# Performance work log

Measured on AMD Instinct MI355X. Metric: run time of the kernel, lower is better.

## Reference

```python
import jax, jax.numpy as jnp
import numpy as np

EPS_BN = 1e-5


def conv2d(x, w, b, stride=1, pad=0):
    y = jax.lax.conv_general_dilated(
        x, w, (stride, stride), [(pad, pad), (pad, pad)],
        dimension_numbers=('NCHW', 'OIHW', 'NCHW'))
    return y + b[None, :, None, None]


def resize_ac(x, oh, ow):
    # bilinear resize, align_corners=True (matches F.interpolate(..., align_corners=True))
    N, C, H, W = x.shape
    ys = jnp.linspace(0.0, H - 1.0, oh)
    xs = jnp.linspace(0.0, W - 1.0, ow)
    y0 = jnp.floor(ys).astype(jnp.int32)
    x0 = jnp.floor(xs).astype(jnp.int32)
    y1 = jnp.minimum(y0 + 1, H - 1)
    x1 = jnp.minimum(x0 + 1, W - 1)
    wy = (ys - y0)[None, None, :, None]
    wx = (xs - x0)[None, None, None, :]
    top = jnp.take(x, y0, axis=2)
    bot = jnp.take(x, y1, axis=2)
    rows = top * (1.0 - wy) + bot * wy
    left = jnp.take(rows, x0, axis=3)
    right = jnp.take(rows, x1, axis=3)
    return left * (1.0 - wx) + right * wx


def grid_sample_3d(vol, grid):
    # vol: (N,C,D,H,W); grid: (N,Do,Ho,Wo,3) with channels (x->W, y->H, z->D)
    # trilinear, padding_mode='zeros', align_corners=False (torch defaults)
    N, C, D, H, W = vol.shape
    out_shape = grid.shape[1:4]
    gx = grid[..., 0].reshape(N, -1)
    gy = grid[..., 1].reshape(N, -1)
    gz = grid[..., 2].reshape(N, -1)
    ix = ((gx + 1.0) * W - 1.0) * 0.5
    iy = ((gy + 1.0) * H - 1.0) * 0.5
    iz = ((gz + 1.0) * D - 1.0) * 0.5
    x0 = jnp.floor(ix); y0 = jnp.floor(iy); z0 = jnp.floor(iz)
    fx = ix - x0; fy = iy - y0; fz = iz - z0
    volf = vol.reshape(N, C, D * H * W)

    def corner(xi, yi, zi, wgt):
        valid = ((xi >= 0) & (xi < W) & (yi >= 0) & (yi < H) & (zi >= 0) & (zi < D))
        xc = jnp.clip(xi, 0, W - 1).astype(jnp.int32)
        yc = jnp.clip(yi, 0, H - 1).astype(jnp.int32)
        zc = jnp.clip(zi, 0, D - 1).astype(jnp.int32)
        lin = (zc * H + yc) * W + xc  # (N,P)
        g = jnp.take_along_axis(volf, lin[:, None, :], axis=2)  # (N,C,P)
        return g * (wgt * valid.astype(vol.dtype))[:, None, :]

    out = 0.0
    for zi, wz in ((z0, 1.0 - fz), (z0 + 1.0, fz)):
        for yi, wy in ((y0, 1.0 - fy), (y0 + 1.0, fy)):
            for xi, wx in ((x0, 1.0 - fx), (x0 + 1.0, fx)):
                out = out + corner(xi, yi, zi, wz * wy * wx)
    return out.reshape(N, C, *out_shape)


def setup_inputs() -> dict:
    key = jax.random.key(0)
    ks = jax.random.split(key, 9)
    N, H, W = 1, 2048, 2048
    f = lambda k, shp, s: jax.random.normal(k, shp, jnp.float32) * s
    return dict(
        low=jax.random.uniform(ks[0], (N, 3, H, W), jnp.float32),
        med=jax.random.uniform(ks[1], (N, 3, H, W), jnp.float32),
        high=jax.random.uniform(ks[2], (N, 3, H, W), jnp.float32),
        w1=f(ks[3], (16, 9, 3, 3), 0.1), b1=jnp.zeros((16,), jnp.float32),
        w2=f(ks[4], (32, 16, 3, 3), 0.1), b2=jnp.zeros((32,), jnp.float32),
        w3=f(ks[5], (64, 32, 3, 3), 0.1), b3=jnp.zeros((64,), jnp.float32),
        w4=f(ks[6], (192, 64, 1, 1), 0.1), b4=jnp.zeros((192,), jnp.float32),
        gw1=f(ks[7], (16, 3, 1, 1), 0.3), gb1=jnp.zeros((16,), jnp.float32),
        g_gamma=jnp.ones((16,), jnp.float32), g_beta=jnp.zeros((16,), jnp.float32),
        g_mean=jnp.zeros((16,), jnp.float32), g_var=jnp.ones((16,), jnp.float32),
        gw2=f(ks[8], (1, 16, 1, 1), 0.3), gb2=jnp.zeros((1,), jnp.float32),
    )


def _forward(low, med, high, w1, b1, w2, b2, w3, b3, w4, b4,
             gw1, gb1, g_gamma, g_beta, g_mean, g_var, gw2, gb2):
    img = 0.33 * low + 0.33 * med + 0.33 * high  # (N,3,H,W)

    # ---- Coeffs: downsample 9-ch input to 128x128, run coeff net -> (N,12,16,16,16)
    x = resize_ac(jnp.concatenate([low, med, high], axis=1), 128, 128)
    x = jax.nn.relu(conv2d(x, w1, b1, stride=2, pad=1))   # 64x64
    x = jax.nn.relu(conv2d(x, w2, b2, stride=2, pad=1))   # 32x32
    x = jax.nn.relu(conv2d(x, w3, b3, stride=2, pad=1))   # 16x16
    coeff = conv2d(x, w4, b4, stride=1, pad=0)            # (N,192,16,16)
    grid_vol = coeff.reshape(-1, 12, 16, 16, 16)          # (N,12,D,H,W)

    # ---- GuideNN at full res: 1x1 conv -> BN(eval) -> ReLU -> 1x1 conv -> sigmoid
    g = conv2d(img, gw1, gb1)
    g = g_gamma[None, :, None, None] * (g - g_mean[None, :, None, None]) \
        * jax.lax.rsqrt(g_var[None, :, None, None] + EPS_BN) + g_beta[None, :, None, None]
    g = jax.nn.relu(g)
    guide = jax.nn.sigmoid(conv2d(g, gw2, gb2))           # (N,1,H,W)
    guide = resize_ac(guide, 64, 64)[:, 0]                # (N,64,64)

    # ---- Slice: trilinear lookup into bilateral grid, guided by (guide, hg, wg)
    N = guide.shape[0]
    lin = (jnp.arange(64, dtype=jnp.float32) / 63.0) * 2.0 - 1.0
    hg = jnp.broadcast_to(lin[:, None], (64, 64))
    wg = jnp.broadcast_to(lin[None, :], (64, 64))
    grid = jnp.stack([guide,
                      jnp.broadcast_to(hg, guide.shape),
                      jnp.broadcast_to(wg, guide.shape)], axis=-1)[:, None]  # (N,1,64,64,3)
    sc = grid_sample_3d(grid_vol, grid)[:, :, 0]          # (N,12,64,64)

    # ---- Apply: upsample coeffs to full res, per-pixel 3x4 affine (HDRNet apply)
    Hi, Wi = img.shape[2], img.shape[3]
    cf = resize_ac(sc, Hi, Wi).reshape(N, 3, 4, Hi, Wi)
    out = jnp.einsum('ncjhw,njhw->nchw', cf[:, :, :3], img) + cf[:, :, 3]
    return out


def reference(low, med, high, w1, b1, w2, b2, w3, b3, w4, b4,
              gw1, gb1, g_gamma, g_beta, g_mean, g_var, gw2, gb2):
    return _forward(low, med, high, w1, b1, w2, b2, w3, b3, w4, b4,
                    gw1, gb1, g_gamma, g_beta, g_mean, g_var, gw2, gb2)
```

## Files before the change

kernel.cpp:

```cpp
#include <hip/hip_runtime.h>
#include <math.h>

#define HH 2048
#define WW 2048
#define HWFULL (HH*WW)

typedef float v4f __attribute__((ext_vector_type(4)));
union F4 { float4 v; v4f c; float f[4]; };

__global__ __launch_bounds__(256) void k_conv1(const float* __restrict__ low,
                                               const float* __restrict__ med,
                                               const float* __restrict__ high,
                                               const float* __restrict__ w,
                                               const float* __restrict__ b,
                                               float* __restrict__ out) {
    __shared__ float sd[9 * 3 * 34];
    const int oy = blockIdx.x >> 2;
    const int q  = blockIdx.x & 3;
    const int tid = threadIdx.x;
    for (int idx = tid; idx < 9 * 3 * 33; idx += 256) {
        int ch = idx / 99;
        int rem = idx - 99 * ch;
        int r = rem / 33;
        int j = rem - 33 * r;
        int ix128 = 32 * q - 1 + j;
        int iy128 = 2 * oy - 1 + r;
        float val = 0.0f;
        if (ix128 >= 0 && ix128 < 128 && iy128 >= 0 && iy128 < 128) {
            const float* base = (ch < 3) ? low : (ch < 6 ? med : high);
            const float* p = base + (ch % 3) * HWFULL;
            float ysf = iy128 * (2047.0f / 127.0f);
            int y0 = (int)ysf; if (y0 > 2047) y0 = 2047;
            int y1 = y0 + 1;   if (y1 > 2047) y1 = 2047;
            float wy = ysf - (float)y0;
            float xsf = ix128 * (2047.0f / 127.0f);
            int x0 = (int)xsf; if (x0 > 2047) x0 = 2047;
            int x1 = x0 + 1;   if (x1 > 2047) x1 = 2047;
            float wx = xsf - (float)x0;
            float t = p[y0 * WW + x0] * (1.0f - wx) + p[y0 * WW + x1] * wx;
            float bo = p[y1 * WW + x0] * (1.0f - wx) + p[y1 * WW + x1] * wx;
            val = t * (1.0f - wy) + bo * wy;
        }
        sd[(ch * 3 + r) * 34 + j] = val;
    }
    __syncthreads();
    int co = tid >> 4, xl = tid & 15;
    float acc = b[co];
    for (int ci = 0; ci < 9; ++ci) {
        #pragma unroll
        for (int ky = 0; ky < 3; ++ky) {
            const float* wr = w + ((co * 9 + ci) * 3 + ky) * 3;
            const float* row = &sd[(ci * 3 + ky) * 34 + 2 * xl];
            acc += wr[0] * row[0] + wr[1] * row[1] + wr[2] * row[2];
        }
    }
    out[co * 4096 + oy * 64 + 16 * q + xl] = fmaxf(acc, 0.0f);
}

__global__ __launch_bounds__(256) void k_conv2(const float* __restrict__ in,
                                               const float* __restrict__ w,
                                               const float* __restrict__ b,
                                               const float* __restrict__ low,
                                               const float* __restrict__ med,
                                               const float* __restrict__ high,
                                               const float* __restrict__ gw1, const float* __restrict__ gb1,
                                               const float* __restrict__ gamma, const float* __restrict__ beta,
                                               const float* __restrict__ mean, const float* __restrict__ var,
                                               const float* __restrict__ gw2, const float* __restrict__ gb2,
                                               float* __restrict__ out,
                                               float* __restrict__ guideb) {
    __shared__ float sd[16 * 3 * 18];
    const int oy = blockIdx.x >> 2;
    const int q  = blockIdx.x & 3;
    const int tid = threadIdx.x;
    for (int idx = tid; idx < 16 * 3 * 17; idx += 256) {
        int ch = idx / 51;
        int rem = idx - 51 * ch;
        int r = rem / 17;
        int j = rem - 17 * r;
        int x = 16 * q - 1 + j;
        int iy = 2 * oy - 1 + r;
        sd[(ch * 3 + r) * 18 + j] =
            (x >= 0 && x < 64 && iy >= 0 && iy < 64) ? in[ch * 4096 + iy * 64 + x] : 0.0f;
    }
    __syncthreads();
    int co = tid >> 3, xl = tid & 7;
    float acc = b[co];
    for (int ci = 0; ci < 16; ++ci) {
        #pragma unroll
        for (int ky = 0; ky < 3; ++ky) {
            const float* wr = w + ((co * 16 + ci) * 3 + ky) * 3;
            const float* row = &sd[(ci * 3 + ky) * 18 + 2 * xl];
            acc += wr[0] * row[0] + wr[1] * row[1] + wr[2] * row[2];
        }
    }
    out[co * 1024 + oy * 32 + 8 * q + xl] = fmaxf(acc, 0.0f);

    if (tid < 32) {
        int g = blockIdx.x * 32 + tid;
        int h = g >> 6, wv = g & 63;
        float ysf = h * (2047.0f / 63.0f);
        int y0 = (int)ysf; if (y0 > 2047) y0 = 2047;
        int y1 = y0 + 1;   if (y1 > 2047) y1 = 2047;
        float wy = ysf - (float)y0;
        float xsf = wv * (2047.0f / 63.0f);
        int x0 = (int)xsf; if (x0 > 2047) x0 = 2047;
        int x1 = x0 + 1;   if (x1 > 2047) x1 = 2047;
        float wx = xsf - (float)x0;
        int yy[2] = { y0, y1 };
        int xx[2] = { x0, x1 };
        float gp[2][2];
        #pragma unroll
        for (int a = 0; a < 2; ++a) {
            #pragma unroll
            for (int bb = 0; bb < 2; ++bb) {
                int pix = yy[a] * WW + xx[bb];
                float i0 = 0.33f * (low[pix]            + med[pix]            + high[pix]);
                float i1 = 0.33f * (low[HWFULL + pix]   + med[HWFULL + pix]   + high[HWFULL + pix]);
                float i2 = 0.33f * (low[2*HWFULL + pix] + med[2*HWFULL + pix] + high[2*HWFULL + pix]);
                float acc2 = gb2[0];
                for (int k = 0; k < 16; ++k) {
                    float t = gb1[k] + gw1[k*3] * i0 + gw1[k*3+1] * i1 + gw1[k*3+2] * i2;
                    t = gamma[k] * (t - mean[k]) * (1.0f / sqrtf(var[k] + 1e-5f)) + beta[k];
                    t = fmaxf(t, 0.0f);
                    acc2 += gw2[k] * t;
                }
                gp[a][bb] = 1.0f / (1.0f + expf(-acc2));
            }
        }
        guideb[g] = (1.0f - wy) * ((1.0f - wx) * gp[0][0] + wx * gp[0][1])
                  +         wy  * ((1.0f - wx) * gp[1][0] + wx * gp[1][1]);
    }
}

__global__ __launch_bounds__(256) void k_conv34(const float* __restrict__ in,
                                                const float* __restrict__ w3,
                                                const float* __restrict__ b3,
                                                const float* __restrict__ w4,
                                                const float* __restrict__ b4,
                                                float* __restrict__ gridvol) {
    __shared__ float sd[32 * 3 * 10];
    __shared__ float sc3[64 * 4];
    const int oy = blockIdx.x >> 2;
    const int q  = blockIdx.x & 3;
    const int tid = threadIdx.x;
    for (int idx = tid; idx < 32 * 3 * 9; idx += 256) {
        int ch = idx / 27;
        int rem = idx - 27 * ch;
        int r = rem / 9;
        int j = rem - 9 * r;
        int x = 8 * q - 1 + j;
        int iy = 2 * oy - 1 + r;
        sd[(ch * 3 + r) * 10 + j] =
            (x >= 0 && x < 32 && iy >= 0 && iy < 32) ? in[ch * 1024 + iy * 32 + x] : 0.0f;
    }
    __syncthreads();
    {
        int co = tid >> 2, xl = tid & 3;
        float acc = b3[co];
        for (int ci = 0; ci < 32; ++ci) {
            #pragma unroll
            for (int ky = 0; ky < 3; ++ky) {
                const float* wr = w3 + ((co * 32 + ci) * 3 + ky) * 3;
                const float* row = &sd[(ci * 3 + ky) * 10 + 2 * xl];
                acc += wr[0] * row[0] + wr[1] * row[1] + wr[2] * row[2];
            }
        }
        sc3[co * 4 + xl] = fmaxf(acc, 0.0f);
    }
    __syncthreads();
    {
        int px = tid & 3;
        int ob = tid >> 2;
        #pragma unroll
        for (int k = 0; k < 3; ++k) {
            int o = ob + 64 * k;
            float sum = b4[o];
            const float* wp = w4 + o * 64;
            for (int i = 0; i < 64; ++i)
                sum += wp[i] * sc3[i * 4 + px];
            gridvol[o * 256 + oy * 16 + 4 * q + px] = sum;
        }
    }
}

__global__ __launch_bounds__(256) void k_slice_ab(
        const float* __restrict__ gridvol, const float* __restrict__ guideb,
        float* __restrict__ ab_full) {
    __shared__ float s[3 * 64 * 12];
    const int b = blockIdx.x;
    const int tid = threadIdx.x;
    float byf = (8 * b) * (63.0f / 2047.0f);
    int v0 = (int)byf; if (v0 > 63) v0 = 63;

    if (tid < 192) {
        int rr = tid >> 6, x = tid & 63;
        int srow = v0 + rr; if (srow > 63) srow = 63;
        float guide = guideb[srow * 64 + x];
        float hg = srow * (2.0f / 63.0f) - 1.0f;
        float wg = x * (2.0f / 63.0f) - 1.0f;
        float ix = ((guide + 1.0f) * 16.0f - 1.0f) * 0.5f;
        float iy = ((hg    + 1.0f) * 16.0f - 1.0f) * 0.5f;
        float iz = ((wg    + 1.0f) * 16.0f - 1.0f) * 0.5f;
        float xf = floorf(ix), yf = floorf(iy), zf = floorf(iz);
        float fx = ix - xf, fyy = iy - yf, fz = iz - zf;
        int xi = (int)xf, yi = (int)yf, zi = (int)zf;
        float scv[12];
        #pragma unroll
        for (int c = 0; c < 12; ++c) scv[c] = 0.0f;
        #pragma unroll
        for (int dz = 0; dz < 2; ++dz) {
            int z = zi + dz; float wz = dz ? fz : 1.0f - fz;
            if (z < 0 || z > 15) continue;
            #pragma unroll
            for (int dy = 0; dy < 2; ++dy) {
                int yv = yi + dy; float wyv = dy ? fyy : 1.0f - fyy;
                if (yv < 0 || yv > 15) continue;
                #pragma unroll
                for (int dx = 0; dx < 2; ++dx) {
                    int xv = xi + dx; float wxv = dx ? fx : 1.0f - fx;
                    if (xv < 0 || xv > 15) continue;
                    float wgt = wz * wyv * wxv;
                    int base = yv * 16 + xv;
                    #pragma unroll
                    for (int c = 0; c < 12; ++c)
                        scv[c] += wgt * gridvol[(c * 16 + z) * 256 + base];
                }
            }
        }
        #pragma unroll
        for (int c = 0; c < 12; ++c) s[(rr * 64 + x) * 12 + c] = scv[c];
    }
    __syncthreads();

    #pragma unroll
    for (int k = 0; k < 24; ++k) {
        int e = k * 256 + tid;
        int r8 = e / 768;
        int rem = e - 768 * r8;
        int x = rem / 12;
        int c = rem - 12 * x;
        int y = 8 * b + r8;
        float iyf = y * (63.0f / 2047.0f);
        int y0 = (int)iyf; if (y0 > 63) y0 = 63;
        int y1 = y0 + 1;   if (y1 > 63) y1 = 63;
        float fy = iyf - (float)y0;
        int i0 = y0 - v0, i1 = y1 - v0;
        float t = s[(i0 * 64 + x) * 12 + c];
        float bo = s[(i1 * 64 + x) * 12 + c];
        ab_full[y * 768 + rem] = t + (bo - t) * fy;
    }
}

__global__ __launch_bounds__(256) void k_apply(
        const float* __restrict__ low, const float* __restrict__ med,
        const float* __restrict__ high, const float* __restrict__ ab_full,
        float* __restrict__ out) {
    __shared__ F4 img[3][512];
    __shared__ F4 abs4[192];
    const int y = blockIdx.x;
    const int tid = threadIdx.x;
    const int HW4 = HWFULL / 4;
    const int base = y << 9;

    const v4f* Lp = (const v4f*)low;
    const v4f* Mp = (const v4f*)med;
    const v4f* Hp = (const v4f*)high;

    if (tid < 192)
        abs4[tid].v = ((const float4*)(ab_full + y * 768))[tid];

    #pragma unroll
    for (int ch = 0; ch < 3; ++ch) {
        int vi = base + ch * HW4 + tid;
        F4 a, b, g, d, e, h;
        a.c = __builtin_nontemporal_load(Lp + vi);
        b.c = __builtin_nontemporal_load(Mp + vi);
        g.c = __builtin_nontemporal_load(Hp + vi);
        d.c = __builtin_nontemporal_load(Lp + vi + 256);
        e.c = __builtin_nontemporal_load(Mp + vi + 256);
        h.c = __builtin_nontemporal_load(Hp + vi + 256);
        F4 r0, r1;
        #pragma unroll
        for (int p = 0; p < 4; ++p) {
            r0.f[p] = 0.33f * (a.f[p] + b.f[p] + g.f[p]);
            r1.f[p] = 0.33f * (d.f[p] + e.f[p] + h.f[p]);
        }
        img[ch][tid] = r0;
        img[ch][tid + 256] = r1;
        __builtin_amdgcn_sched_barrier(0);
    }
    __syncthreads();

    v4f* Op = (v4f*)out;
    #pragma unroll
    for (int q = 0; q < 2; ++q) {
        int v = tid + q * 256;
        int vi = base + v;
        int x_first = v << 2;
        float ixf0 = x_first * (63.0f / 2047.0f);
        int f = (int)ixf0; if (f > 63) f = 63;
        float ixf3 = (x_first + 3) * (63.0f / 2047.0f);
        int s3 = (int)ixf3; if (s3 > 63) s3 = 63;
        int fp1 = f + 1;  if (fp1 > 63) fp1 = 63;
        int sp1 = s3 + 1; if (sp1 > 63) sp1 = 63;
        F4 A0[3], B0[3], C0[3];
        #pragma unroll
        for (int qq = 0; qq < 3; ++qq) {
            A0[qq] = abs4[f   * 3 + qq];
            B0[qq] = abs4[fp1 * 3 + qq];
            C0[qq] = abs4[sp1 * 3 + qq];
        }
        F4 i0 = img[0][v], i1 = img[1][v], i2 = img[2][v];

        F4 o0, o1, o2;
        #pragma unroll
        for (int p = 0; p < 4; ++p) {
            int x = x_first + p;
            float ixf = x * (63.0f / 2047.0f);
            int x0 = (int)ixf; if (x0 > 63) x0 = 63;
            float fx = ixf - (float)x0;
            bool first = (x0 == f);
            float cf[12];
            #pragma unroll
            for (int qq = 0; qq < 3; ++qq) {
                #pragma unroll
                for (int r = 0; r < 4; ++r) {
                    float a = first ? A0[qq].f[r] : B0[qq].f[r];
                    float bb = first ? B0[qq].f[r] : C0[qq].f[r];
                    cf[qq * 4 + r] = a + (bb - a) * fx;
                }
            }
            o0.f[p] = cf[0] * i0.f[p] + cf[1]  * i1.f[p] + cf[2]  * i2.f[p] + cf[3];
            o1.f[p] = cf[4] * i0.f[p] + cf[5]  * i1.f[p] + cf[6]  * i2.f[p] + cf[7];
            o2.f[p] = cf[8] * i0.f[p] + cf[9]  * i1.f[p] + cf[10] * i2.f[p] + cf[11];
        }
        __builtin_nontemporal_store(o0.c, Op + vi);
        __builtin_nontemporal_store(o1.c, Op + vi + HW4);
        __builtin_nontemporal_store(o2.c, Op + vi + 2 * HW4);
    }
}

extern "C" void kernel_launch(void* const* d_in, const int* in_sizes, int n_in,
                              void* d_out, int out_size, void* d_ws, size_t ws_size,
                              hipStream_t stream) {
    const float* low   = (const float*)d_in[0];
    const float* med   = (const float*)d_in[1];
    const float* high  = (const float*)d_in[2];
    const float* w1    = (const float*)d_in[3];
    const float* b1    = (const float*)d_in[4];
    const float* w2    = (const float*)d_in[5];
    const float* b2    = (const float*)d_in[6];
    const float* w3    = (const float*)d_in[7];
    const float* b3    = (const float*)d_in[8];
    const float* w4    = (const float*)d_in[9];
    const float* b4    = (const float*)d_in[10];
    const float* gw1   = (const float*)d_in[11];
    const float* gb1   = (const float*)d_in[12];
    const float* gamma = (const float*)d_in[13];
    const float* beta  = (const float*)d_in[14];
    const float* mean  = (const float*)d_in[15];
    const float* var   = (const float*)d_in[16];
    const float* gw2   = (const float*)d_in[17];
    const float* gb2   = (const float*)d_in[18];
    float* out = (float*)d_out;

    float* ws      = (float*)d_ws;
    float* ab_full = ws;
    float* c1      = ab_full + 1572864;
    float* c2v     = c1 + 65536;
    float* gridvol = c2v + 32768;
    float* guideb  = gridvol + 49152;

    hipLaunchKernelGGL(k_conv1,    dim3(256), dim3(256), 0, stream,
                       low, med, high, w1, b1, c1);
    hipLaunchKernelGGL(k_conv2,    dim3(128), dim3(256), 0, stream,
                       c1, w2, b2, low, med, high,
                       gw1, gb1, gamma, beta, mean, var, gw2, gb2, c2v, guideb);
    hipLaunchKernelGGL(k_conv34,   dim3(64),  dim3(256), 0, stream, c2v, w3, b3, w4, b4, gridvol);
    hipLaunchKernelGGL(k_slice_ab, dim3(256), dim3(256), 0, stream, gridvol, guideb, ab_full);
    hipLaunchKernelGGL(k_apply,    dim3(2048), dim3(256), 0, stream, low, med, high, ab_full, out);
}
```

Baseline: 87.33 us.

## Stage full input rows per wavefront plane into LDS with 512-thread apply blocks

The apply kernel now uses 512 threads per row. Each wavefront loads one whole input plane row (eight of the nine plane rows) into a 9x2048 shared buffer, using a rotated chunk order, and all threads together load the ninth plane. The old per-channel interleaved loads across the three images are gone, and each thread computes one output vec4 instead of two. The goal is more memory-level parallelism and contiguous per-wave streams, at the cost of about 73KB of LDS per block, which may limit occupancy.

```diff
diff --git a/kernel.cpp b/kernel.cpp
--- a/kernel.cpp
+++ b/kernel.cpp
@@ -252,93 +252,98 @@
     }
 }
 
-__global__ __launch_bounds__(256) void k_apply(
+__global__ __launch_bounds__(512) void k_apply(
         const float* __restrict__ low, const float* __restrict__ med,
         const float* __restrict__ high, const float* __restrict__ ab_full,
         float* __restrict__ out) {
-    __shared__ F4 img[3][512];
+    __shared__ float sP[9][2048];
     __shared__ F4 abs4[192];
     const int y = blockIdx.x;
     const int tid = threadIdx.x;
+    const int lane = tid & 63;
+    const int w = tid >> 6;
     const int HW4 = HWFULL / 4;
-    const int base = y << 9;
-
-    const v4f* Lp = (const v4f*)low;
-    const v4f* Mp = (const v4f*)med;
-    const v4f* Hp = (const v4f*)high;
 
     if (tid < 192)
         abs4[tid].v = ((const float4*)(ab_full + y * 768))[tid];
 
+    const float* plane =
+        (w < 3 ? low + w * HWFULL :
+         w < 6 ? med + (w - 3) * HWFULL :
+                 high + (w - 6) * HWFULL) + y * WW;
+
     #pragma unroll
-    for (int ch = 0; ch < 3; ++ch) {
-        int vi = base + ch * HW4 + tid;
-        F4 a, b, g, d, e, h;
-        a.c = __builtin_nontemporal_load(Lp + vi);
-        b.c = __builtin_nontemporal_load(Mp + vi);
-        g.c = __builtin_nontemporal_load(Hp + vi);
-        d.c = __builtin_nontemporal_load(Lp + vi + 256);
-        e.c = __builtin_nontemporal_load(Mp + vi + 256);
-        h.c = __builtin_nontemporal_load(Hp + vi + 256);
-        F4 r0, r1;
+    for (int i = 0; i < 8; ++i) {
+        int off = (((w + i) & 7) << 8) + (lane << 2);
+        F4 t;
+        t.c = __builtin_nontemporal_load((const v4f*)(plane + off));
+        *(F4*)&sP[w][off] = t;
+    }
+    {
+        const float* p8 = high + 2 * HWFULL + y * WW;
+        int off = tid << 2;
+        F4 t;
+        t.c = __builtin_nontemporal_load((const v4f*)(p8 + off));
+        *(F4*)&sP[8][off] = t;
+    }
+    __syncthreads();
+
+    const int v = tid;
+    const int vi = (y << 9) + v;
+    F4 i0, i1, i2;
+    {
+        F4 a0 = *(F4*)&sP[0][v << 2], a1 = *(F4*)&sP[3][v << 2], a2 = *(F4*)&sP[6][v << 2];
+        F4 b0 = *(F4*)&sP[1][v << 2], b1 = *(F4*)&sP[4][v << 2], b2 = *(F4*)&sP[7][v << 2];
+        F4 c0 = *(F4*)&sP[2][v << 2], c1 = *(F4*)&sP[5][v << 2], c2 = *(F4*)&sP[8][v << 2];
         #pragma unroll
         for (int p = 0; p < 4; ++p) {
-            r0.f[p] = 0.33f * (a.f[p] + b.f[p] + g.f[p]);
-            r1.f[p] = 0.33f * (d.f[p] + e.f[p] + h.f[p]);
-        }
-        img[ch][tid] = r0;
-        img[ch][tid + 256] = r1;
-        __builtin_amdgcn_sched_barrier(0);
-    }
-    __syncthreads();
-
+            i0.f[p] = 0.33f * (a0.f[p] + a1.f[p] + a2.f[p]);
+            i1.f[p] = 0.33f * (b0.f[p] + b1.f[p] + b2.f[p]);
+            i2.f[p] = 0.33f * (c0.f[p] + c1.f[p] + c2.f[p]);
+        }
+    }
+
+    int x_first = v << 2;
+    float ixf0 = x_first * (63.0f / 2047.0f);
+    int f = (int)ixf0; if (f > 63) f = 63;
+    float ixf3 = (x_first + 3) * (63.0f / 2047.0f);
+    int s3 = (int)ixf3; if (s3 > 63) s3 = 63;
+    int fp1 = f + 1;  if (fp1 > 63) fp1 = 63;
+    int sp1 = s3 + 1; if (sp1 > 63) sp1 = 63;
+    F4 A0[3], B0[3], C0[3];
+    #pragma unroll
+    for (int qq = 0; qq < 3; ++qq) {
+        A0[qq] = abs4[f   * 3 + qq];
+        B0[qq] = abs4[fp1 * 3 + qq];
+        C0[qq] = abs4[sp1 * 3 + qq];
+    }
+
+    F4 o0, o1, o2;
+    #pragma unroll
+    for (int p = 0; p < 4; ++p) {
+        int x = x_first + p;
+        float ixf = x * (63.0f / 2047.0f);
+        int x0 = (int)ixf; if (x0 > 63) x0 = 63;
+        float fx = ixf - (float)x0;
+        bool first = (x0 == f);
+        float cf[12];
+        #pragma unroll
+        for (int qq = 0; qq < 3; ++qq) {
+            #pragma unroll
+            for (int r = 0; r < 4; ++r) {
+                float a = first ? A0[qq].f[r] : B0[qq].f[r];
+                float bb = first ? B0[qq].f[r] : C0[qq].f[r];
+                cf[qq * 4 + r] = a + (bb - a) * fx;
+            }
+        }
+        o0.f[p] = cf[0] * i0.f[p] + cf[1]  * i1.f[p] + cf[2]  * i2.f[p] + cf[3];
+        o1.f[p] = cf[4] * i0.f[p] + cf[5]  * i1.f[p] + cf[6]  * i2.f[p] + cf[7];
+        o2.f[p] = cf[8] * i0.f[p] + cf[9]  * i1.f[p] + cf[10] * i2.f[p] + cf[11];
+    }
     v4f* Op = (v4f*)out;
-    #pragma unroll
-    for (int q = 0; q < 2; ++q) {
-        int v = tid + q * 256;
-        int vi = base + v;
-        int x_first = v << 2;
-        float ixf0 = x_first * (63.0f / 2047.0f);
-        int f = (int)ixf0; if (f > 63) f = 63;
-        float ixf3 = (x_first + 3) * (63.0f / 2047.0f);
-        int s3 = (int)ixf3; if (s3 > 63) s3 = 63;
-        int fp1 = f + 1;  if (fp1 > 63) fp1 = 63;
-        int sp1 = s3 + 1; if (sp1 > 63) sp1 = 63;
-        F4 A0[3], B0[3], C0[3];
-        #pragma unroll
-        for (int qq = 0; qq < 3; ++qq) {
-            A0[qq] = abs4[f   * 3 + qq];
-            B0[qq] = abs4[fp1 * 3 + qq];
-            C0[qq] = abs4[sp1 * 3 + qq];
-        }
-        F4 i0 = img[0][v], i1 = img[1][v], i2 = img[2][v];
-
-        F4 o0, o1, o2;
-        #pragma unroll
-        for (int p = 0; p < 4; ++p) {
-            int x = x_first + p;
-            float ixf = x * (63.0f / 2047.0f);
-            int x0 = (int)ixf; if (x0 > 63) x0 = 63;
-            float fx = ixf - (float)x0;
-            bool first = (x0 == f);
-            float cf[12];
-            #pragma unroll
-            for (int qq = 0; qq < 3; ++qq) {
-                #pragma unroll
-                for (int r = 0; r < 4; ++r) {
-                    float a = first ? A0[qq].f[r] : B0[qq].f[r];
-                    float bb = first ? B0[qq].f[r] : C0[qq].f[r];
-                    cf[qq * 4 + r] = a + (bb - a) * fx;
-                }
-            }
-            o0.f[p] = cf[0] * i0.f[p] + cf[1]  * i1.f[p] + cf[2]  * i2.f[p] + cf[3];
-            o1.f[p] = cf[4] * i0.f[p] + cf[5]  * i1.f[p] + cf[6]  * i2.f[p] + cf[7];
-            o2.f[p] = cf[8] * i0.f[p] + cf[9]  * i1.f[p] + cf[10] * i2.f[p] + cf[11];
-        }
-        __builtin_nontemporal_store(o0.c, Op + vi);
-        __builtin_nontemporal_store(o1.c, Op + vi + HW4);
-        __builtin_nontemporal_store(o2.c, Op + vi + 2 * HW4);
-    }
+    __builtin_nontemporal_store(o0.c, Op + vi);
+    __builtin_nontemporal_store(o1.c, Op + vi + HW4);
+    __builtin_nontemporal_store(o2.c, Op + vi + 2 * HW4);
 }
 
 extern "C" void kernel_launch(void* const* d_in, const int* in_sizes, int n_in,
@@ -379,5 +384,5 @@
                        gw1, gb1, gamma, beta, mean, var, gw2, gb2, c2v, guideb);
     hipLaunchKernelGGL(k_conv34,   dim3(64),  dim3(256), 0, stream, c2v, w3, b3, w4, b4, gridvol);
     hipLaunchKernelGGL(k_slice_ab, dim3(256), dim3(256), 0, stream, gridvol, guideb, ab_full);
-    hipLaunchKernelGGL(k_apply,    dim3(2048), dim3(256), 0, stream, low, med, high, ab_full, out);
-}
+    hipLaunchKernelGGL(k_apply,    dim3(2048), dim3(512), 0, stream, low, med, high, ab_full, out);
+}
```

After: 88.37 us. No clear change (+1.2%).
